# Kernel optimization log

Hardware: AMD Instinct MI355X
Metric: run time of the kernel (lower is better)

The kernel has to match this reference:

```python
import jax, jax.numpy as jnp
import numpy as np

EPS = 1e-12

def softmax_mask(x, mask, axis):
    # stable masked softmax: exp(x - max) * mask / (sum + eps)
    shift = jnp.max(x, axis=axis, keepdims=True)
    e = jnp.exp(x - shift) * mask
    return e / (jnp.sum(e, axis=axis, keepdims=True) + EPS)

def setup_inputs() -> dict:
    key = jax.random.key(0)
    kq, kk, kv, km = jax.random.split(key, 4)
    B, Lq, Lk, d, dv = 16, 2048, 2048, 128, 128
    q = jax.random.normal(kq, (B, Lq, d), dtype=jnp.float32)
    k = jax.random.normal(kk, (B, Lk, d), dtype=jnp.float32)
    v = jax.random.normal(kv, (B, Lk, dv), dtype=jnp.float32)
    mask = (jax.random.uniform(km, (B, Lq, Lk)) > 0.1).astype(jnp.float32)
    return {"q": q, "k": k, "v": v, "mask": mask}

def reference(q, k, v, mask):
    # attn[b,i,j] = q[b,i,:] . k[b,j,:]
    attn = jnp.einsum('bqd,bkd->bqk', q, k)
    col_attn = softmax_mask(attn, mask, axis=1)  # normalize over queries (columns)
    row_attn = softmax_mask(attn, mask, axis=2)  # normalize over keys (rows)
    gated = col_attn * row_attn
    output = jnp.einsum('bqk,bkd->bqd', gated, v)
    return (output, gated)
```

## Files before the change

kernel.cpp:

```cpp
#include <hip/hip_runtime.h>

#define BATCH 16
#define LSEQ  2048
#define DDIM  128
#define EPSV  1e-12f
#define NTILE (LSEQ / 64)
#define NROWS (BATCH * LSEQ)
#define MASKED_NEG (-1e30f)

typedef __attribute__((ext_vector_type(4))) float f32x4;
typedef __attribute__((ext_vector_type(8))) __bf16 bf16x8;
typedef __attribute__((ext_vector_type(8))) unsigned short u16x8;

__device__ __forceinline__ unsigned short f2bf(float x) {
    unsigned int u = __float_as_uint(x);
    u += 0x7FFFu + ((u >> 16) & 1u);
    return (unsigned short)(u >> 16);
}
__device__ __forceinline__ float bf2f(unsigned short h) {
    return __uint_as_float(((unsigned int)h) << 16);
}

__device__ __forceinline__ int swz(int row, int col8) {
    return (row << 6) + ((((col8 >> 3) ^ row) & 7) << 3);
}

__device__ __forceinline__ void gll16(const unsigned short* src, unsigned short* ldsdst) {
    __builtin_amdgcn_global_load_lds(
        (const __attribute__((address_space(1))) void*)src,
        (__attribute__((address_space(3))) void*)ldsdst, 16, 0, 0);
}

__global__ __launch_bounds__(256) void k0_split(
    const float* __restrict__ q, const float* __restrict__ kmat,
    unsigned short* __restrict__ qh, unsigned short* __restrict__ ql,
    unsigned short* __restrict__ kh, unsigned short* __restrict__ kl)
{
    const float* s     = blockIdx.y ? kmat : q;
    unsigned short* ph = blockIdx.y ? kh : qh;
    unsigned short* pl = blockIdx.y ? kl : ql;
    const size_t i = ((size_t)blockIdx.x * 256 + threadIdx.x) << 3;
    float xs[8];
    *(float4*)&xs[0] = *(const float4*)(s + i);
    *(float4*)&xs[4] = *(const float4*)(s + i + 4);
    u16x8 hh, ll;
#pragma unroll
    for (int e = 0; e < 8; ++e) {
        const unsigned short h = f2bf(xs[e]);
        hh[e] = h;
        ll[e] = f2bf(xs[e] - bf2f(h));
    }
    *(u16x8*)(ph + i) = hh;
    *(u16x8*)(pl + i) = ll;
}

__global__ __launch_bounds__(256) void k0_vtrans(
    const float* __restrict__ v,
    unsigned short* __restrict__ vth, unsigned short* __restrict__ vtl)
{
    const int b  = blockIdx.z;
    const int j0 = blockIdx.x * 64;
    const int d0 = blockIdx.y * 64;
    __shared__ float T[64][65];

    const int tid = threadIdx.x;
    {
        const int jr = tid >> 4;
        const int c4 = (tid & 15) << 2;
#pragma unroll
        for (int p = 0; p < 4; ++p) {
            const int row = jr + (p << 4);
            *(float4*)&T[row][c4] =
                *(const float4*)(v + ((size_t)b * LSEQ + j0 + row) * DDIM + d0 + c4);
        }
    }
    __syncthreads();

    const int dr = tid >> 2;
    const int jc = (tid & 3) << 4;
    u16x8 h[2], l[2];
#pragma unroll
    for (int e = 0; e < 16; ++e) {
        const float x = T[jc + e][dr];
        const unsigned short hh = f2bf(x);
        h[e >> 3][e & 7] = hh;
        l[e >> 3][e & 7] = f2bf(x - bf2f(hh));
    }
    unsigned short* oh = vth + ((size_t)b * DDIM + d0 + dr) * LSEQ + j0 + jc;
    unsigned short* ol = vtl + ((size_t)b * DDIM + d0 + dr) * LSEQ + j0 + jc;
    *(u16x8*)oh = h[0]; *(u16x8*)(oh + 8) = h[1];
    *(u16x8*)ol = l[0]; *(u16x8*)(ol + 8) = l[1];
}

__global__ __launch_bounds__(256, 2) void k1_qk_stats(
    const unsigned short* __restrict__ qh, const unsigned short* __restrict__ ql,
    const unsigned short* __restrict__ kh, const unsigned short* __restrict__ kl,
    const float* __restrict__ mask, float* __restrict__ attn,
    float* __restrict__ rowMt, float* __restrict__ rowSt,
    float* __restrict__ colMt, float* __restrict__ colSt)
{
    const int b  = blockIdx.z;
    const int it = blockIdx.y * 128;
    const int jt = blockIdx.x * 128;

    __shared__ __attribute__((aligned(16))) unsigned short smem[4 * 128 * 64];
    unsigned short* Ah = smem;
    unsigned short* Al = smem + 8192;
    unsigned short* Bh = smem + 16384;
    unsigned short* Bl = smem + 24576;

    const int tid  = threadIdx.x;
    const int lane = tid & 63;
    const int w    = tid >> 6;
    const int wrow = (w >> 1) << 6;
    const int wcol = (w & 1) << 6;
    const int g    = lane >> 4;
    const int cl   = lane & 15;

    const unsigned short* splane = (w == 0) ? qh : (w == 1) ? ql : (w == 2) ? kh : kl;
    const size_t srow0 = (size_t)b * LSEQ + ((w < 2) ? it : jt);
    unsigned short* dplane = smem + w * 8192;
    const int srow = lane >> 3;
    const int sslt = lane & 7;

    f32x4 acc[4][4];
    const f32x4 zero = {0.f, 0.f, 0.f, 0.f};
#pragma unroll
    for (int i = 0; i < 4; ++i)
#pragma unroll
        for (int j = 0; j < 4; ++j) acc[i][j] = zero;

    float mreg[4][4][4];
    const float* mrow = mask + ((size_t)b * LSEQ + it + wrow) * LSEQ + jt + wcol;

#pragma unroll
    for (int half = 0; half < 2; ++half) {
        const int ks2 = half << 6;
        if (half) __syncthreads();
#pragma unroll
        for (int qq = 0; qq < 16; ++qq) {
            const int row = (qq << 3) + srow;
            const int ss  = sslt ^ (row & 7);
            gll16(splane + (srow0 + row) * DDIM + ks2 + (ss << 3),
                  dplane + (qq << 9));
        }
        if (half) {
#pragma unroll
            for (int fr = 0; fr < 4; ++fr)
#pragma unroll
                for (int r = 0; r < 4; ++r)
#pragma unroll
                    for (int fc = 0; fc < 4; ++fc)
                        mreg[fr][r][fc] =
                            mrow[(size_t)((fr << 4) + (g << 2) + r) * LSEQ + (fc << 4) + cl];
        }
        __syncthreads();

#pragma unroll
        for (int ks = 0; ks < 64; ks += 32) {
            const int colb = ks + (g << 3);
            bf16x8 ah[4], al[4], bh[4], bl[4];
#pragma unroll
            for (int f = 0; f < 4; ++f) {
                const int ra = wrow + (f << 4) + cl;
                const int rb = wcol + (f << 4) + cl;
                ah[f] = __builtin_bit_cast(bf16x8, *(const u16x8*)&Ah[swz(ra, colb)]);
                al[f] = __builtin_bit_cast(bf16x8, *(const u16x8*)&Al[swz(ra, colb)]);
                bh[f] = __builtin_bit_cast(bf16x8, *(const u16x8*)&Bh[swz(rb, colb)]);
                bl[f] = __builtin_bit_cast(bf16x8, *(const u16x8*)&Bl[swz(rb, colb)]);
            }
#pragma unroll
            for (int fr = 0; fr < 4; ++fr)
#pragma unroll
                for (int fc = 0; fc < 4; ++fc) {
                    acc[fr][fc] = __builtin_amdgcn_mfma_f32_16x16x32_bf16(ah[fr], bh[fc], acc[fr][fc], 0, 0, 0);
                    acc[fr][fc] = __builtin_amdgcn_mfma_f32_16x16x32_bf16(ah[fr], bl[fc], acc[fr][fc], 0, 0, 0);
                    acc[fr][fc] = __builtin_amdgcn_mfma_f32_16x16x32_bf16(al[fr], bh[fc], acc[fr][fc], 0, 0, 0);
                }
        }
    }

    float* arow = attn + ((size_t)b * LSEQ + it + wrow) * LSEQ + jt + wcol;

    float colm[4];
#pragma unroll
    for (int fc = 0; fc < 4; ++fc) {
        float m = acc[0][fc][0];
#pragma unroll
        for (int fr = 0; fr < 4; ++fr)
#pragma unroll
            for (int r = 0; r < 4; ++r) m = fmaxf(m, acc[fr][fc][r]);
        m = fmaxf(m, __shfl_xor(m, 16, 64));
        m = fmaxf(m, __shfl_xor(m, 32, 64));
        colm[fc] = m;
    }
    float rowm[4][4];
#pragma unroll
    for (int fr = 0; fr < 4; ++fr)
#pragma unroll
        for (int r = 0; r < 4; ++r) {
            float m = fmaxf(fmaxf(acc[fr][0][r], acc[fr][1][r]),
                            fmaxf(acc[fr][2][r], acc[fr][3][r]));
            m = fmaxf(m, __shfl_xor(m, 1, 64));
            m = fmaxf(m, __shfl_xor(m, 2, 64));
            m = fmaxf(m, __shfl_xor(m, 4, 64));
            m = fmaxf(m, __shfl_xor(m, 8, 64));
            rowm[fr][r] = m;
        }

    float cols_[4] = {0.f, 0.f, 0.f, 0.f};
    float rows_[4][4];
#pragma unroll
    for (int fr = 0; fr < 4; ++fr) {
#pragma unroll
        for (int r = 0; r < 4; ++r) {
            const int R = (fr << 4) + (g << 2) + r;
            const float rm = rowm[fr][r];
            float rs = 0.f;
#pragma unroll
            for (int fc = 0; fc < 4; ++fc) {
                const int C = (fc << 4) + cl;
                const float x  = acc[fr][fc][r];
                const float xp = (mreg[fr][r][fc] != 0.f) ? x : MASKED_NEG;
                arow[(size_t)R * LSEQ + C] = xp;
                rs        += __expf(xp - rm);
                cols_[fc] += __expf(xp - colm[fc]);
            }
            rs += __shfl_xor(rs, 1, 64);
            rs += __shfl_xor(rs, 2, 64);
            rs += __shfl_xor(rs, 4, 64);
            rs += __shfl_xor(rs, 8, 64);
            rows_[fr][r] = rs;
        }
    }
#pragma unroll
    for (int fc = 0; fc < 4; ++fc) {
        float s = cols_[fc];
        s += __shfl_xor(s, 16, 64);
        s += __shfl_xor(s, 32, 64);
        cols_[fc] = s;
    }

    const int ti = (blockIdx.y << 1) + (w >> 1);
    const int tj = (blockIdx.x << 1) + (w & 1);
    if (cl == 0) {
        const size_t rbase = (size_t)tj * NROWS + (size_t)b * LSEQ + it + wrow;
#pragma unroll
        for (int fr = 0; fr < 4; ++fr)
#pragma unroll
            for (int r = 0; r < 4; ++r) {
                const int R = (fr << 4) + (g << 2) + r;
                rowMt[rbase + R] = rowm[fr][r];
                rowSt[rbase + R] = rows_[fr][r];
            }
    }
    if (g == 0) {
        const size_t cbase = (size_t)ti * NROWS + (size_t)b * LSEQ + jt + wcol;
#pragma unroll
        for (int fc = 0; fc < 4; ++fc) {
            colMt[cbase + (fc << 4) + cl] = colm[fc];
            colSt[cbase + (fc << 4) + cl] = cols_[fc];
        }
    }
}

__global__ __launch_bounds__(256) void k2_combine(
    const float* __restrict__ rowMt, const float* __restrict__ rowSt,
    const float* __restrict__ colMt, const float* __restrict__ colSt,
    float* __restrict__ rmaxf, float* __restrict__ rinvf,
    float* __restrict__ cmaxf, float* __restrict__ cinvf)
{
    const int id = blockIdx.x * 256 + threadIdx.x;
    const bool isRow = (id < NROWS);
    const int off = isRow ? id : id - NROWS;
    const float* Mt = isRow ? rowMt : colMt;
    const float* St = isRow ? rowSt : colSt;

    float m = -INFINITY;
#pragma unroll
    for (int t = 0; t < NTILE; ++t) m = fmaxf(m, Mt[(size_t)t * NROWS + off]);
    float s = 0.f;
#pragma unroll
    for (int t = 0; t < NTILE; ++t)
        s += St[(size_t)t * NROWS + off] * __expf(Mt[(size_t)t * NROWS + off] - m);
    const float inv = 1.f / (s + EPSV);

    if (isRow) { rmaxf[off] = m; rinvf[off] = inv; }
    else       { cmaxf[off] = m; cinvf[off] = inv; }
}

__global__ __launch_bounds__(256, 3) void k3_gated_out(
    const unsigned short* __restrict__ vth, const unsigned short* __restrict__ vtl,
    const float* __restrict__ rmaxf, const float* __restrict__ cmaxf,
    const float* __restrict__ rinvf, const float* __restrict__ cinvf,
    float* __restrict__ gated, float* __restrict__ outp)
{
    const int b   = blockIdx.y;
    const int it0 = blockIdx.x * 32;

    __shared__ __attribute__((aligned(16))) unsigned short Gh[32 * 64];
    __shared__ __attribute__((aligned(16))) unsigned short Gl[32 * 64];
    __shared__ __attribute__((aligned(16))) unsigned short Vh[128 * 64];
    __shared__ __attribute__((aligned(16))) unsigned short Vl[128 * 64];

    const int tid  = threadIdx.x;
    const int lane = tid & 63;
    const int w    = tid >> 6;
    const int g    = lane >> 4;
    const int cl   = lane & 15;

    const int grow = tid >> 3;
    const int gcb  = (tid & 7) << 3;

    const float mrw = rmaxf[b * LSEQ + it0 + grow];
    const float irw = rinvf[b * LSEQ + it0 + grow];

    float* gb = gated + ((size_t)b * LSEQ + it0) * LSEQ;

    unsigned short* vplane_d       = (w >> 1) ? Vl : Vh;
    const unsigned short* vplane_s = (w >> 1) ? vtl : vth;
    const int vrow0 = (w & 1) << 6;
    const int srow  = lane >> 3;
    const int sslt  = lane & 7;

    f32x4 acc[2][2];
    const f32x4 zero = {0.f, 0.f, 0.f, 0.f};
#pragma unroll
    for (int i = 0; i < 2; ++i) { acc[i][0] = zero; acc[i][1] = zero; }

    float4 xn[2], cmn[2], cin[2];
#pragma unroll
    for (int p = 0; p < 2; ++p) {
        xn[p]  = *(const float4*)(gb + (size_t)grow * LSEQ + gcb + (p << 2));
        cmn[p] = *(const float4*)(cmaxf + b * LSEQ + gcb + (p << 2));
        cin[p] = *(const float4*)(cinvf + b * LSEQ + gcb + (p << 2));
    }

#pragma unroll 1
    for (int j0 = 0; j0 < LSEQ; j0 += 64) {
        __syncthreads();
#pragma unroll
        for (int qq = 0; qq < 8; ++qq) {
            const int row = vrow0 + (qq << 3) + srow;
            const int ss  = sslt ^ (row & 7);
            gll16(vplane_s + ((size_t)b * DDIM + row) * LSEQ + j0 + (ss << 3),
                  vplane_d + (((vrow0 >> 3) + qq) << 9));
        }

        float4 xc[2], cmc[2], cic[2];
#pragma unroll
        for (int p = 0; p < 2; ++p) { xc[p] = xn[p]; cmc[p] = cmn[p]; cic[p] = cin[p]; }
        if (j0 + 64 < LSEQ) {
#pragma unroll
            for (int p = 0; p < 2; ++p) {
                xn[p]  = *(const float4*)(gb + (size_t)grow * LSEQ + j0 + 64 + gcb + (p << 2));
                cmn[p] = *(const float4*)(cmaxf + b * LSEQ + j0 + 64 + gcb + (p << 2));
                cin[p] = *(const float4*)(cinvf + b * LSEQ + j0 + 64 + gcb + (p << 2));
            }
        }

        float gs[8];
#pragma unroll
        for (int p = 0; p < 2; ++p) {
            const float xs[4]  = {xc[p].x, xc[p].y, xc[p].z, xc[p].w};
            const float cms[4] = {cmc[p].x, cmc[p].y, cmc[p].z, cmc[p].w};
            const float cis[4] = {cic[p].x, cic[p].y, cic[p].z, cic[p].w};
#pragma unroll
            for (int e = 0; e < 4; ++e)
                gs[(p << 2) + e] = __expf(2.f * xs[e] - mrw - cms[e]) * irw * cis[e];
            *(float4*)(gb + (size_t)grow * LSEQ + j0 + gcb + (p << 2)) =
                make_float4(gs[(p << 2)], gs[(p << 2) + 1], gs[(p << 2) + 2], gs[(p << 2) + 3]);
        }
        u16x8 hh, ll;
#pragma unroll
        for (int e = 0; e < 8; ++e) {
            const unsigned short hb = f2bf(gs[e]);
            hh[e] = hb;
            ll[e] = f2bf(gs[e] - bf2f(hb));
        }
        *(u16x8*)&Gh[swz(grow, gcb)] = hh;
        *(u16x8*)&Gl[swz(grow, gcb)] = ll;

        __syncthreads();

#pragma unroll
        for (int ks = 0; ks < 64; ks += 32) {
            const int colb = ks + (g << 3);
            bf16x8 ah[2], al[2], bh[2], bl[2];
#pragma unroll
            for (int f = 0; f < 2; ++f) {
                const int ra = (f << 4) + cl;
                ah[f] = __builtin_bit_cast(bf16x8, *(const u16x8*)&Gh[swz(ra, colb)]);
                al[f] = __builtin_bit_cast(bf16x8, *(const u16x8*)&Gl[swz(ra, colb)]);
                const int rb = (w << 5) + (f << 4) + cl;
                bh[f] = __builtin_bit_cast(bf16x8, *(const u16x8*)&Vh[swz(rb, colb)]);
                bl[f] = __builtin_bit_cast(bf16x8, *(const u16x8*)&Vl[swz(rb, colb)]);
            }
#pragma unroll
            for (int fr = 0; fr < 2; ++fr)
#pragma unroll
                for (int fc = 0; fc < 2; ++fc) {
                    acc[fr][fc] = __builtin_amdgcn_mfma_f32_16x16x32_bf16(ah[fr], bh[fc], acc[fr][fc], 0, 0, 0);
                    acc[fr][fc] = __builtin_amdgcn_mfma_f32_16x16x32_bf16(al[fr], bh[fc], acc[fr][fc], 0, 0, 0);
                    acc[fr][fc] = __builtin_amdgcn_mfma_f32_16x16x32_bf16(ah[fr], bl[fc], acc[fr][fc], 0, 0, 0);
                }
        }
    }

    float* ob = outp + ((size_t)b * LSEQ + it0) * DDIM + (w << 5);
#pragma unroll
    for (int fr = 0; fr < 2; ++fr)
#pragma unroll
        for (int r = 0; r < 4; ++r) {
            const int R = (fr << 4) + (g << 2) + r;
#pragma unroll
            for (int fc = 0; fc < 2; ++fc)
                ob[(size_t)R * DDIM + (fc << 4) + cl] = acc[fr][fc][r];
        }
}

extern "C" void kernel_launch(void* const* d_in, const int* in_sizes, int n_in,
                              void* d_out, int out_size, void* d_ws, size_t ws_size,
                              hipStream_t stream)
{
    (void)in_sizes; (void)n_in; (void)out_size; (void)ws_size;
    const float* q    = (const float*)d_in[0];
    const float* k    = (const float*)d_in[1];
    const float* v    = (const float*)d_in[2];
    const float* mask = (const float*)d_in[3];

    float* outp  = (float*)d_out;
    float* gated = (float*)d_out + (size_t)BATCH * LSEQ * DDIM;

    float* rowMt = (float*)d_ws;
    float* rowSt = rowMt + (size_t)NTILE * NROWS;
    float* colMt = rowSt + (size_t)NTILE * NROWS;
    float* colSt = colMt + (size_t)NTILE * NROWS;
    float* rmaxf = colSt + (size_t)NTILE * NROWS;
    float* rinvf = rmaxf + NROWS;
    float* cmaxf = rinvf + NROWS;
    float* cinvf = cmaxf + NROWS;
    unsigned short* vth = (unsigned short*)(cinvf + NROWS);
    unsigned short* vtl = vth + (size_t)BATCH * DDIM * LSEQ;
    unsigned short* qhp = vtl + (size_t)BATCH * DDIM * LSEQ;
    unsigned short* qlp = qhp + (size_t)BATCH * LSEQ * DDIM;
    unsigned short* khp = qlp + (size_t)BATCH * LSEQ * DDIM;
    unsigned short* klp = khp + (size_t)BATCH * LSEQ * DDIM;

    dim3 gsplit((BATCH * LSEQ * DDIM) / 2048, 2);
    k0_split<<<gsplit, dim3(256), 0, stream>>>(q, k, qhp, qlp, khp, klp);

    dim3 g0(LSEQ / 64, DDIM / 64, BATCH);
    k0_vtrans<<<g0, dim3(256), 0, stream>>>(v, vth, vtl);

    dim3 g1(LSEQ / 128, LSEQ / 128, BATCH);
    k1_qk_stats<<<g1, dim3(256), 0, stream>>>(qhp, qlp, khp, klp, mask, gated,
                                              rowMt, rowSt, colMt, colSt);

    k2_combine<<<dim3(2 * NROWS / 256), dim3(256), 0, stream>>>(
        rowMt, rowSt, colMt, colSt, rmaxf, rinvf, cmaxf, cinvf);

    dim3 g3(LSEQ / 32, BATCH);
    k3_gated_out<<<g3, dim3(256), 0, stream>>>(vth, vtl, rmaxf, cmaxf,
                                               rinvf, cinvf, gated, outp);
}
```

Baseline: 693.5 us.

## Recompute QK^T in gated pass and pack mask to bits instead of storing attn

Adds a kernel that packs the float mask into 64-bit ballot words. The stats kernel then reads mask bits and no longer writes the masked attention matrix to global memory. The final kernel recomputes the QK^T tile with split-bf16 MFMAs before forming the gated weights and multiplying by V, and now handles 64 query rows per block instead of 32. This trades a full write and read of the B×L×L fp32 intermediate for redoing the QK GEMM plus extra LDS traffic. It also drops the occupancy hint on k3.

```diff
diff --git a/kernel.cpp b/kernel.cpp
--- a/kernel.cpp
+++ b/kernel.cpp
@@ -6,6 +6,7 @@
 #define EPSV  1e-12f
 #define NTILE (LSEQ / 64)
 #define NROWS (BATCH * LSEQ)
+#define NWORD (LSEQ / 64)
 #define MASKED_NEG (-1e30f)
 
 typedef __attribute__((ext_vector_type(4))) float f32x4;
@@ -19,10 +20,6 @@
 }
 __device__ __forceinline__ float bf2f(unsigned short h) {
     return __uint_as_float(((unsigned int)h) << 16);
-}
-
-__device__ __forceinline__ int swz(int row, int col8) {
-    return (row << 6) + ((((col8 >> 3) ^ row) & 7) << 3);
 }
 
 __device__ __forceinline__ void gll16(const unsigned short* src, unsigned short* ldsdst) {
@@ -92,10 +89,26 @@
     *(u16x8*)ol = l[0]; *(u16x8*)(ol + 8) = l[1];
 }
 
+__global__ __launch_bounds__(256) void k0_pack(
+    const float* __restrict__ mask, unsigned long long* __restrict__ bits)
+{
+    const int tid  = threadIdx.x;
+    const int lane = tid & 63;
+    const int w    = tid >> 6;
+    const size_t row = (size_t)blockIdx.x * 4 + w;
+    const float* mr = mask + row * LSEQ;
+    unsigned long long* br = bits + row * NWORD;
+#pragma unroll 4
+    for (int j = 0; j < LSEQ; j += 64) {
+        const unsigned long long m = __ballot(mr[j + lane] != 0.f);
+        if (lane == 0) br[j >> 6] = m;
+    }
+}
+
 __global__ __launch_bounds__(256, 2) void k1_qk_stats(
     const unsigned short* __restrict__ qh, const unsigned short* __restrict__ ql,
     const unsigned short* __restrict__ kh, const unsigned short* __restrict__ kl,
-    const float* __restrict__ mask, float* __restrict__ attn,
+    const unsigned long long* __restrict__ bits,
     float* __restrict__ rowMt, float* __restrict__ rowSt,
     float* __restrict__ colMt, float* __restrict__ colSt)
 {
@@ -130,9 +143,6 @@
 #pragma unroll
         for (int j = 0; j < 4; ++j) acc[i][j] = zero;
 
-    float mreg[4][4][4];
-    const float* mrow = mask + ((size_t)b * LSEQ + it + wrow) * LSEQ + jt + wcol;
-
 #pragma unroll
     for (int half = 0; half < 2; ++half) {
         const int ks2 = half << 6;
@@ -144,16 +154,6 @@
             gll16(splane + (srow0 + row) * DDIM + ks2 + (ss << 3),
                   dplane + (qq << 9));
         }
-        if (half) {
-#pragma unroll
-            for (int fr = 0; fr < 4; ++fr)
-#pragma unroll
-                for (int r = 0; r < 4; ++r)
-#pragma unroll
-                    for (int fc = 0; fc < 4; ++fc)
-                        mreg[fr][r][fc] =
-                            mrow[(size_t)((fr << 4) + (g << 2) + r) * LSEQ + (fc << 4) + cl];
-        }
         __syncthreads();
 
 #pragma unroll
@@ -164,10 +164,12 @@
             for (int f = 0; f < 4; ++f) {
                 const int ra = wrow + (f << 4) + cl;
                 const int rb = wcol + (f << 4) + cl;
-                ah[f] = __builtin_bit_cast(bf16x8, *(const u16x8*)&Ah[swz(ra, colb)]);
-                al[f] = __builtin_bit_cast(bf16x8, *(const u16x8*)&Al[swz(ra, colb)]);
-                bh[f] = __builtin_bit_cast(bf16x8, *(const u16x8*)&Bh[swz(rb, colb)]);
-                bl[f] = __builtin_bit_cast(bf16x8, *(const u16x8*)&Bl[swz(rb, colb)]);
+                const int oa = (ra << 6) + ((((colb >> 3) ^ ra) & 7) << 3);
+                const int ob = (rb << 6) + ((((colb >> 3) ^ rb) & 7) << 3);
+                ah[f] = __builtin_bit_cast(bf16x8, *(const u16x8*)&Ah[oa]);
+                al[f] = __builtin_bit_cast(bf16x8, *(const u16x8*)&Al[oa]);
+                bh[f] = __builtin_bit_cast(bf16x8, *(const u16x8*)&Bh[ob]);
+                bl[f] = __builtin_bit_cast(bf16x8, *(const u16x8*)&Bl[ob]);
             }
 #pragma unroll
             for (int fr = 0; fr < 4; ++fr)
@@ -180,7 +182,13 @@
         }
     }
 
-    float* arow = attn + ((size_t)b * LSEQ + it + wrow) * LSEQ + jt + wcol;
+    unsigned long long wb[4][4];
+#pragma unroll
+    for (int fr = 0; fr < 4; ++fr)
+#pragma unroll
+        for (int r = 0; r < 4; ++r)
+            wb[fr][r] = bits[((size_t)b * LSEQ + it + wrow + (fr << 4) + (g << 2) + r)
+                             * NWORD + ((jt + wcol) >> 6)];
 
     float colm[4];
 #pragma unroll
@@ -214,15 +222,12 @@
     for (int fr = 0; fr < 4; ++fr) {
 #pragma unroll
         for (int r = 0; r < 4; ++r) {
-            const int R = (fr << 4) + (g << 2) + r;
             const float rm = rowm[fr][r];
             float rs = 0.f;
 #pragma unroll
             for (int fc = 0; fc < 4; ++fc) {
-                const int C = (fc << 4) + cl;
                 const float x  = acc[fr][fc][r];
-                const float xp = (mreg[fr][r][fc] != 0.f) ? x : MASKED_NEG;
-                arow[(size_t)R * LSEQ + C] = xp;
+                const float xp = ((wb[fr][r] >> ((fc << 4) + cl)) & 1ULL) ? x : MASKED_NEG;
                 rs        += __expf(xp - rm);
                 cols_[fc] += __expf(xp - colm[fc]);
             }
@@ -289,19 +294,24 @@
     else       { cmaxf[off] = m; cinvf[off] = inv; }
 }
 
-__global__ __launch_bounds__(256, 3) void k3_gated_out(
+__global__ __launch_bounds__(256) void k3_gated_out(
+    const unsigned short* __restrict__ qh, const unsigned short* __restrict__ ql,
+    const unsigned short* __restrict__ kh, const unsigned short* __restrict__ kl,
     const unsigned short* __restrict__ vth, const unsigned short* __restrict__ vtl,
+    const unsigned long long* __restrict__ bits,
     const float* __restrict__ rmaxf, const float* __restrict__ cmaxf,
     const float* __restrict__ rinvf, const float* __restrict__ cinvf,
     float* __restrict__ gated, float* __restrict__ outp)
 {
     const int b   = blockIdx.y;
-    const int it0 = blockIdx.x * 32;
-
-    __shared__ __attribute__((aligned(16))) unsigned short Gh[32 * 64];
-    __shared__ __attribute__((aligned(16))) unsigned short Gl[32 * 64];
-    __shared__ __attribute__((aligned(16))) unsigned short Vh[128 * 64];
-    __shared__ __attribute__((aligned(16))) unsigned short Vl[128 * 64];
+    const int it0 = blockIdx.x * 64;
+
+    __shared__ __attribute__((aligned(16))) unsigned short Kh_[64 * 128];
+    __shared__ __attribute__((aligned(16))) unsigned short Kl_[64 * 128];
+    __shared__ __attribute__((aligned(16))) unsigned short Vh_[128 * 64];
+    __shared__ __attribute__((aligned(16))) unsigned short Vl_[128 * 64];
+    __shared__ __attribute__((aligned(16))) unsigned short Gh_[64 * 64];
+    __shared__ __attribute__((aligned(16))) unsigned short Gl_[64 * 64];
 
     const int tid  = threadIdx.x;
     const int lane = tid & 63;
@@ -309,113 +319,140 @@
     const int g    = lane >> 4;
     const int cl   = lane & 15;
 
-    const int grow = tid >> 3;
-    const int gcb  = (tid & 7) << 3;
-
-    const float mrw = rmaxf[b * LSEQ + it0 + grow];
-    const float irw = rinvf[b * LSEQ + it0 + grow];
-
-    float* gb = gated + ((size_t)b * LSEQ + it0) * LSEQ;
-
-    unsigned short* vplane_d       = (w >> 1) ? Vl : Vh;
-    const unsigned short* vplane_s = (w >> 1) ? vtl : vth;
-    const int vrow0 = (w & 1) << 6;
-    const int srow  = lane >> 3;
-    const int sslt  = lane & 7;
-
-    f32x4 acc[2][2];
+#pragma unroll
+    for (int p = 0; p < 4; ++p) {
+        const int op  = (w << 2) + p;
+        const int row = (op << 2) + (lane >> 4);
+        const int ss  = (lane & 15) ^ (row & 15);
+        gll16(qh + ((size_t)b * LSEQ + it0 + row) * DDIM + (ss << 3), Kh_ + (op << 9));
+        gll16(ql + ((size_t)b * LSEQ + it0 + row) * DDIM + (ss << 3), Kl_ + (op << 9));
+    }
+    __syncthreads();
+
+    bf16x8 aqh[4], aql[4];
+    {
+        const int row = (w << 4) + cl;
+#pragma unroll
+        for (int ks = 0; ks < 4; ++ks) {
+            const int slt = (((ks << 2) + g) ^ (row & 15));
+            aqh[ks] = __builtin_bit_cast(bf16x8, *(const u16x8*)&Kh_[(row << 7) + (slt << 3)]);
+            aql[ks] = __builtin_bit_cast(bf16x8, *(const u16x8*)&Kl_[(row << 7) + (slt << 3)]);
+        }
+    }
+    float mrw[4], irw[4];
+#pragma unroll
+    for (int r = 0; r < 4; ++r) {
+        const int R = it0 + (w << 4) + (g << 2) + r;
+        mrw[r] = rmaxf[b * LSEQ + R];
+        irw[r] = rinvf[b * LSEQ + R];
+    }
+
+    f32x4 oacc[4][2];
     const f32x4 zero = {0.f, 0.f, 0.f, 0.f};
 #pragma unroll
-    for (int i = 0; i < 2; ++i) { acc[i][0] = zero; acc[i][1] = zero; }
-
-    float4 xn[2], cmn[2], cin[2];
-#pragma unroll
-    for (int p = 0; p < 2; ++p) {
-        xn[p]  = *(const float4*)(gb + (size_t)grow * LSEQ + gcb + (p << 2));
-        cmn[p] = *(const float4*)(cmaxf + b * LSEQ + gcb + (p << 2));
-        cin[p] = *(const float4*)(cinvf + b * LSEQ + gcb + (p << 2));
-    }
+    for (int qf = 0; qf < 4; ++qf) { oacc[qf][0] = zero; oacc[qf][1] = zero; }
+
+    __syncthreads();
 
 #pragma unroll 1
     for (int j0 = 0; j0 < LSEQ; j0 += 64) {
+#pragma unroll
+        for (int p = 0; p < 4; ++p) {
+            const int op = (w << 2) + p;
+            const int rk = (op << 2) + (lane >> 4);
+            const int sk = (lane & 15) ^ (rk & 15);
+            gll16(kh + ((size_t)b * LSEQ + j0 + rk) * DDIM + (sk << 3), Kh_ + (op << 9));
+            gll16(kl + ((size_t)b * LSEQ + j0 + rk) * DDIM + (sk << 3), Kl_ + (op << 9));
+            const int rv = (op << 3) + (lane >> 3);
+            const int sv = (lane & 7) ^ (rv & 7);
+            gll16(vth + ((size_t)b * DDIM + rv) * LSEQ + j0 + (sv << 3), Vh_ + (op << 9));
+            gll16(vtl + ((size_t)b * DDIM + rv) * LSEQ + j0 + (sv << 3), Vl_ + (op << 9));
+        }
         __syncthreads();
-#pragma unroll
-        for (int qq = 0; qq < 8; ++qq) {
-            const int row = vrow0 + (qq << 3) + srow;
-            const int ss  = sslt ^ (row & 7);
-            gll16(vplane_s + ((size_t)b * DDIM + row) * LSEQ + j0 + (ss << 3),
-                  vplane_d + (((vrow0 >> 3) + qq) << 9));
-        }
-
-        float4 xc[2], cmc[2], cic[2];
-#pragma unroll
-        for (int p = 0; p < 2; ++p) { xc[p] = xn[p]; cmc[p] = cmn[p]; cic[p] = cin[p]; }
-        if (j0 + 64 < LSEQ) {
-#pragma unroll
-            for (int p = 0; p < 2; ++p) {
-                xn[p]  = *(const float4*)(gb + (size_t)grow * LSEQ + j0 + 64 + gcb + (p << 2));
-                cmn[p] = *(const float4*)(cmaxf + b * LSEQ + j0 + 64 + gcb + (p << 2));
-                cin[p] = *(const float4*)(cinvf + b * LSEQ + j0 + 64 + gcb + (p << 2));
-            }
-        }
-
-        float gs[8];
-#pragma unroll
-        for (int p = 0; p < 2; ++p) {
-            const float xs[4]  = {xc[p].x, xc[p].y, xc[p].z, xc[p].w};
-            const float cms[4] = {cmc[p].x, cmc[p].y, cmc[p].z, cmc[p].w};
-            const float cis[4] = {cic[p].x, cic[p].y, cic[p].z, cic[p].w};
-#pragma unroll
-            for (int e = 0; e < 4; ++e)
-                gs[(p << 2) + e] = __expf(2.f * xs[e] - mrw - cms[e]) * irw * cis[e];
-            *(float4*)(gb + (size_t)grow * LSEQ + j0 + gcb + (p << 2)) =
-                make_float4(gs[(p << 2)], gs[(p << 2) + 1], gs[(p << 2) + 2], gs[(p << 2) + 3]);
-        }
-        u16x8 hh, ll;
-#pragma unroll
-        for (int e = 0; e < 8; ++e) {
-            const unsigned short hb = f2bf(gs[e]);
-            hh[e] = hb;
-            ll[e] = f2bf(gs[e] - bf2f(hb));
-        }
-        *(u16x8*)&Gh[swz(grow, gcb)] = hh;
-        *(u16x8*)&Gl[swz(grow, gcb)] = ll;
-
+
+        f32x4 xacc[4];
+#pragma unroll
+        for (int jf = 0; jf < 4; ++jf) xacc[jf] = zero;
+#pragma unroll
+        for (int ks = 0; ks < 4; ++ks) {
+            bf16x8 bh[4], bl[4];
+#pragma unroll
+            for (int jf = 0; jf < 4; ++jf) {
+                const int rb  = (jf << 4) + cl;
+                const int slt = (((ks << 2) + g) ^ (rb & 15));
+                bh[jf] = __builtin_bit_cast(bf16x8, *(const u16x8*)&Kh_[(rb << 7) + (slt << 3)]);
+                bl[jf] = __builtin_bit_cast(bf16x8, *(const u16x8*)&Kl_[(rb << 7) + (slt << 3)]);
+            }
+#pragma unroll
+            for (int jf = 0; jf < 4; ++jf) {
+                xacc[jf] = __builtin_amdgcn_mfma_f32_16x16x32_bf16(aqh[ks], bh[jf], xacc[jf], 0, 0, 0);
+                xacc[jf] = __builtin_amdgcn_mfma_f32_16x16x32_bf16(aqh[ks], bl[jf], xacc[jf], 0, 0, 0);
+                xacc[jf] = __builtin_amdgcn_mfma_f32_16x16x32_bf16(aql[ks], bh[jf], xacc[jf], 0, 0, 0);
+            }
+        }
+
+        unsigned long long wb[4];
+#pragma unroll
+        for (int r = 0; r < 4; ++r)
+            wb[r] = bits[((size_t)b * LSEQ + it0 + (w << 4) + (g << 2) + r) * NWORD + (j0 >> 6)];
+        float* gbase = gated + ((size_t)b * LSEQ + it0 + (w << 4) + (g << 2)) * LSEQ + j0;
+#pragma unroll
+        for (int jf = 0; jf < 4; ++jf) {
+            const int c = (jf << 4) + cl;
+            const float cmv = cmaxf[b * LSEQ + j0 + c];
+            const float civ = cinvf[b * LSEQ + j0 + c];
+#pragma unroll
+            for (int r = 0; r < 4; ++r) {
+                const float x  = xacc[jf][r];
+                const float xp = ((wb[r] >> c) & 1ULL) ? x : MASKED_NEG;
+                const float gv = __expf(2.f * xp - mrw[r] - cmv) * irw[r] * civ;
+                gbase[(size_t)r * LSEQ + c] = gv;
+                const unsigned short hb = f2bf(gv);
+                const unsigned short lb = f2bf(gv - bf2f(hb));
+                const int grow = (w << 4) + (g << 2) + r;
+                const int gidx = (grow << 6) + (((((jf << 1) + (cl >> 3)) ^ grow) & 7) << 3) + (cl & 7);
+                Gh_[gidx] = hb;
+                Gl_[gidx] = lb;
+            }
+        }
         __syncthreads();
 
 #pragma unroll
-        for (int ks = 0; ks < 64; ks += 32) {
-            const int colb = ks + (g << 3);
-            bf16x8 ah[2], al[2], bh[2], bl[2];
-#pragma unroll
-            for (int f = 0; f < 2; ++f) {
-                const int ra = (f << 4) + cl;
-                ah[f] = __builtin_bit_cast(bf16x8, *(const u16x8*)&Gh[swz(ra, colb)]);
-                al[f] = __builtin_bit_cast(bf16x8, *(const u16x8*)&Gl[swz(ra, colb)]);
-                const int rb = (w << 5) + (f << 4) + cl;
-                bh[f] = __builtin_bit_cast(bf16x8, *(const u16x8*)&Vh[swz(rb, colb)]);
-                bl[f] = __builtin_bit_cast(bf16x8, *(const u16x8*)&Vl[swz(rb, colb)]);
-            }
-#pragma unroll
-            for (int fr = 0; fr < 2; ++fr)
-#pragma unroll
-                for (int fc = 0; fc < 2; ++fc) {
-                    acc[fr][fc] = __builtin_amdgcn_mfma_f32_16x16x32_bf16(ah[fr], bh[fc], acc[fr][fc], 0, 0, 0);
-                    acc[fr][fc] = __builtin_amdgcn_mfma_f32_16x16x32_bf16(al[fr], bh[fc], acc[fr][fc], 0, 0, 0);
-                    acc[fr][fc] = __builtin_amdgcn_mfma_f32_16x16x32_bf16(ah[fr], bl[fc], acc[fr][fc], 0, 0, 0);
+        for (int kc = 0; kc < 2; ++kc) {
+            bf16x8 agh[4], agl[4];
+#pragma unroll
+            for (int qf = 0; qf < 4; ++qf) {
+                const int ra  = (qf << 4) + cl;
+                const int slt = (((kc << 2) + g) ^ (ra & 7));
+                agh[qf] = __builtin_bit_cast(bf16x8, *(const u16x8*)&Gh_[(ra << 6) + (slt << 3)]);
+                agl[qf] = __builtin_bit_cast(bf16x8, *(const u16x8*)&Gl_[(ra << 6) + (slt << 3)]);
+            }
+#pragma unroll
+            for (int nf = 0; nf < 2; ++nf) {
+                const int rb  = (w << 5) + (nf << 4) + cl;
+                const int slt = (((kc << 2) + g) ^ (rb & 7));
+                const bf16x8 bvh = __builtin_bit_cast(bf16x8, *(const u16x8*)&Vh_[(rb << 6) + (slt << 3)]);
+                const bf16x8 bvl = __builtin_bit_cast(bf16x8, *(const u16x8*)&Vl_[(rb << 6) + (slt << 3)]);
+#pragma unroll
+                for (int qf = 0; qf < 4; ++qf) {
+                    oacc[qf][nf] = __builtin_amdgcn_mfma_f32_16x16x32_bf16(agh[qf], bvh, oacc[qf][nf], 0, 0, 0);
+                    oacc[qf][nf] = __builtin_amdgcn_mfma_f32_16x16x32_bf16(agl[qf], bvh, oacc[qf][nf], 0, 0, 0);
+                    oacc[qf][nf] = __builtin_amdgcn_mfma_f32_16x16x32_bf16(agh[qf], bvl, oacc[qf][nf], 0, 0, 0);
                 }
-        }
+            }
+        }
+        __syncthreads();
     }
 
     float* ob = outp + ((size_t)b * LSEQ + it0) * DDIM + (w << 5);
 #pragma unroll
-    for (int fr = 0; fr < 2; ++fr)
+    for (int qf = 0; qf < 4; ++qf)
 #pragma unroll
         for (int r = 0; r < 4; ++r) {
-            const int R = (fr << 4) + (g << 2) + r;
-#pragma unroll
-            for (int fc = 0; fc < 2; ++fc)
-                ob[(size_t)R * DDIM + (fc << 4) + cl] = acc[fr][fc][r];
+            const int R = (qf << 4) + (g << 2) + r;
+#pragma unroll
+            for (int nf = 0; nf < 2; ++nf)
+                ob[(size_t)R * DDIM + (nf << 4) + cl] = oacc[qf][nf][r];
         }
 }
 
@@ -432,7 +469,8 @@
     float* outp  = (float*)d_out;
     float* gated = (float*)d_out + (size_t)BATCH * LSEQ * DDIM;
 
-    float* rowMt = (float*)d_ws;
+    unsigned long long* bitsw = (unsigned long long*)d_ws;
+    float* rowMt = (float*)(bitsw + (size_t)NROWS * NWORD);
     float* rowSt = rowMt + (size_t)NTILE * NROWS;
     float* colMt = rowSt + (size_t)NTILE * NROWS;
     float* colSt = colMt + (size_t)NTILE * NROWS;
@@ -453,14 +491,17 @@
     dim3 g0(LSEQ / 64, DDIM / 64, BATCH);
     k0_vtrans<<<g0, dim3(256), 0, stream>>>(v, vth, vtl);
 
+    k0_pack<<<dim3(NROWS / 4), dim3(256), 0, stream>>>(mask, bitsw);
+
     dim3 g1(LSEQ / 128, LSEQ / 128, BATCH);
-    k1_qk_stats<<<g1, dim3(256), 0, stream>>>(qhp, qlp, khp, klp, mask, gated,
+    k1_qk_stats<<<g1, dim3(256), 0, stream>>>(qhp, qlp, khp, klp, bitsw,
                                               rowMt, rowSt, colMt, colSt);
 
     k2_combine<<<dim3(2 * NROWS / 256), dim3(256), 0, stream>>>(
         rowMt, rowSt, colMt, colSt, rmaxf, rinvf, cmaxf, cinvf);
 
-    dim3 g3(LSEQ / 32, BATCH);
-    k3_gated_out<<<g3, dim3(256), 0, stream>>>(vth, vtl, rmaxf, cmaxf,
-                                               rinvf, cinvf, gated, outp);
-}
+    dim3 g3(LSEQ / 64, BATCH);
+    k3_gated_out<<<g3, dim3(256), 0, stream>>>(qhp, qlp, khp, klp, vth, vtl, bitsw,
+                                               rmaxf, cmaxf, rinvf, cinvf,
+                                               gated, outp);
+}
```

New measurement: 844.1 us. +21.7%, slower.
